# Optimization experiments

Measured on AMD Instinct MI355X. Metric: run time of the kernel, lower is better.

## Reference

```python
import jax, jax.numpy as jnp
import numpy as np

B, X_DIM, Y_DIM, HIDDEN = 512, 768, 128, 1024
H2 = HIDDEN // 2


def setup_inputs() -> dict:
    key = jax.random.key(0)
    ks = jax.random.split(key, 10)
    s_in = 1.0 / np.sqrt(X_DIM)
    s_h = 1.0 / np.sqrt(H2)
    return {
        "x_samples": jax.random.normal(ks[0], (B, X_DIM), jnp.float32),
        "y_samples": jax.random.normal(ks[1], (B, Y_DIM), jnp.float32),
        "w1_mu": jax.random.uniform(ks[2], (X_DIM, H2), jnp.float32, -s_in, s_in),
        "b1_mu": jax.random.uniform(ks[3], (H2,), jnp.float32, -s_in, s_in),
        "w2_mu": jax.random.uniform(ks[4], (H2, Y_DIM), jnp.float32, -s_h, s_h),
        "b2_mu": jax.random.uniform(ks[5], (Y_DIM,), jnp.float32, -s_h, s_h),
        "w1_lv": jax.random.uniform(ks[6], (X_DIM, H2), jnp.float32, -s_in, s_in),
        "b1_lv": jax.random.uniform(ks[7], (H2,), jnp.float32, -s_in, s_in),
        "w2_lv": jax.random.uniform(ks[8], (H2, Y_DIM), jnp.float32, -s_h, s_h),
        "b2_lv": jax.random.uniform(ks[9], (Y_DIM,), jnp.float32, -s_h, s_h),
    }


def reference(x_samples, y_samples, w1_mu, b1_mu, w2_mu, b2_mu,
              w1_lv, b1_lv, w2_lv, b2_lv):
    batch = y_samples.shape[0]
    # p_mu / p_logvar MLP heads
    mu = jax.nn.relu(x_samples @ w1_mu + b1_mu) @ w2_mu + b2_mu          # [B, Y]
    logvar = jnp.tanh(jax.nn.relu(x_samples @ w1_lv + b1_lv) @ w2_lv + b2_lv)  # [B, Y]

    inv_var = jnp.exp(-logvar)
    # positive: diagonal Gaussian log-prob of y_i under p(.|x_i), up to const
    positive = (-0.5 * (mu - y_samples) ** 2 * inv_var - 0.5 * logvar).sum(-1)  # [B]

    # pairwise log-probs: row i = params from x_i, col j = sample y_j
    mu_1 = mu[:, None, :]            # [B, 1, Y]
    lv_1 = logvar[:, None, :]        # [B, 1, Y]
    y_1 = y_samples[None, :, :]      # [1, B, Y]
    all_probs = (-0.5 * (y_1 - mu_1) ** 2 * jnp.exp(-lv_1) - 0.5 * lv_1).sum(-1)  # [B, B]

    # Faithful replication of the torch broadcasting: diag_mask is [B, B, 1],
    # so all_probs + diag_mask broadcasts to [B, B, B], then logsumexp over dim 0.
    diag_mask = (jnp.eye(batch, dtype=all_probs.dtype) * -20.0)[:, :, None]  # [B, B, 1]
    logits = all_probs + diag_mask                                           # [B, B, B]
    negative = jax.scipy.special.logsumexp(logits, axis=0) - jnp.log(batch - 1.0)  # [B, B]

    return (positive - negative).mean()
```

## Files before the change

### kernel.cpp

```cpp
#include <hip/hip_runtime.h>
#include <math.h>

#define BSZ   512
#define XD    768
#define YD    128
#define H2D   512

__global__ __launch_bounds__(512) void ysum_kernel(
    const float* __restrict__ y, double* __restrict__ Sy,
    double* __restrict__ Sy2, double* __restrict__ accum)
{
    const int t  = threadIdx.x;
    const int dl = t & 31;
    const int g  = t >> 5;
    const int d  = blockIdx.x * 32 + dl;

    float s = 0.f, s2 = 0.f;
    for (int i = g * 32; i < g * 32 + 32; ++i) {
        const float v = y[i * YD + d];
        s += v; s2 += v * v;
    }
    __shared__ float sh[16][33];
    __shared__ float sh2[16][33];
    sh[g][dl] = s; sh2[g][dl] = s2;
    __syncthreads();
    if (t < 32) {
        double S = 0.0, S2 = 0.0;
        #pragma unroll
        for (int gg = 0; gg < 16; ++gg) { S += (double)sh[gg][t]; S2 += (double)sh2[gg][t]; }
        Sy[blockIdx.x * 32 + t]  = S;
        Sy2[blockIdx.x * 32 + t] = S2;
    } else if (blockIdx.x == 0 && t == 32) {
        accum[0] = 0.0;
    } else if (blockIdx.x == 0 && t == 33) {
        accum[1] = 0.0;
    }
}

__global__ __launch_bounds__(256, 2) void layer1_kernel(
    const float* __restrict__ x,
    const float* __restrict__ w1_mu, const float* __restrict__ b1_mu,
    const float* __restrict__ w1_lv, const float* __restrict__ b1_lv,
    float* __restrict__ h_mu, float* __restrict__ h_lv)
{
    const int which = blockIdx.z;
    const float* __restrict__ W    = which ? w1_lv : w1_mu;
    const float* __restrict__ bias = which ? b1_lv : b1_mu;
    float* __restrict__ H          = which ? h_lv  : h_mu;

    __shared__ float As[32][68];
    __shared__ float Bs[32][68];

    const int t  = threadIdx.x;
    const int m0 = blockIdx.x * 32;
    const int n0 = blockIdx.y * 32;
    const int tx = t & 15;
    const int ty = t >> 4;

    const int ar = t >> 3;
    const int ak = (t & 7) * 8;
    const int bk = t >> 2;
    const int bn = (t & 3) * 8;

    float acc00 = 0.f, acc01 = 0.f, acc10 = 0.f, acc11 = 0.f;

    for (int k0 = 0; k0 < XD; k0 += 64) {
        const float4 a_lo = *(const float4*)&x[(m0 + ar) * XD + k0 + ak];
        const float4 a_hi = *(const float4*)&x[(m0 + ar) * XD + k0 + ak + 4];
        const float4 w_lo = *(const float4*)&W[(k0 + bk) * H2D + n0 + bn];
        const float4 w_hi = *(const float4*)&W[(k0 + bk) * H2D + n0 + bn + 4];
        __syncthreads();
        *(float4*)&As[ar][ak]     = a_lo;
        *(float4*)&As[ar][ak + 4] = a_hi;
        Bs[bn + 0][bk] = w_lo.x; Bs[bn + 1][bk] = w_lo.y;
        Bs[bn + 2][bk] = w_lo.z; Bs[bn + 3][bk] = w_lo.w;
        Bs[bn + 4][bk] = w_hi.x; Bs[bn + 5][bk] = w_hi.y;
        Bs[bn + 6][bk] = w_hi.z; Bs[bn + 7][bk] = w_hi.w;
        __syncthreads();
        #pragma unroll
        for (int k = 0; k < 64; k += 4) {
            const float4 a0 = *(const float4*)&As[ty][k];
            const float4 a1 = *(const float4*)&As[ty + 16][k];
            const float4 b0 = *(const float4*)&Bs[tx][k];
            const float4 b1 = *(const float4*)&Bs[tx + 16][k];
            acc00 += a0.x*b0.x; acc00 += a0.y*b0.y; acc00 += a0.z*b0.z; acc00 += a0.w*b0.w;
            acc01 += a0.x*b1.x; acc01 += a0.y*b1.y; acc01 += a0.z*b1.z; acc01 += a0.w*b1.w;
            acc10 += a1.x*b0.x; acc10 += a1.y*b0.y; acc10 += a1.z*b0.z; acc10 += a1.w*b0.w;
            acc11 += a1.x*b1.x; acc11 += a1.y*b1.y; acc11 += a1.z*b1.z; acc11 += a1.w*b1.w;
        }
    }

    const int na = n0 + tx, nb = n0 + tx + 16;
    const float ba = bias[na], bb = bias[nb];
    H[(m0 + ty)      * H2D + na] = fmaxf(acc00 + ba, 0.f);
    H[(m0 + ty)      * H2D + nb] = fmaxf(acc01 + bb, 0.f);
    H[(m0 + ty + 16) * H2D + na] = fmaxf(acc10 + ba, 0.f);
    H[(m0 + ty + 16) * H2D + nb] = fmaxf(acc11 + bb, 0.f);
}

__global__ __launch_bounds__(256, 2) void layer2p_kernel(
    const float* __restrict__ h_mu, const float* __restrict__ h_lv,
    const float* __restrict__ w2_mu, const float* __restrict__ w2_lv,
    float* __restrict__ part)
{
    const int branch = blockIdx.z >> 2;
    const int kz     = blockIdx.z & 3;
    const float* __restrict__ A = branch ? h_lv  : h_mu;
    const float* __restrict__ W = branch ? w2_lv : w2_mu;
    float* __restrict__ out = part + (size_t)blockIdx.z * (BSZ * YD);

    __shared__ float As[32][68];
    __shared__ float Bs[32][68];

    const int t  = threadIdx.x;
    const int m0 = blockIdx.x * 32;
    const int n0 = blockIdx.y * 32;
    const int tx = t & 15;
    const int ty = t >> 4;

    const int ar = t >> 3;
    const int ak = (t & 7) * 8;
    const int bk = t >> 2;
    const int bn = (t & 3) * 8;

    float acc00 = 0.f, acc01 = 0.f, acc10 = 0.f, acc11 = 0.f;

    const int kbase = kz * 128;
    for (int k0 = kbase; k0 < kbase + 128; k0 += 64) {
        const float4 a_lo = *(const float4*)&A[(m0 + ar) * H2D + k0 + ak];
        const float4 a_hi = *(const float4*)&A[(m0 + ar) * H2D + k0 + ak + 4];
        const float4 w_lo = *(const float4*)&W[(k0 + bk) * YD + n0 + bn];
        const float4 w_hi = *(const float4*)&W[(k0 + bk) * YD + n0 + bn + 4];
        __syncthreads();
        *(float4*)&As[ar][ak]     = a_lo;
        *(float4*)&As[ar][ak + 4] = a_hi;
        Bs[bn + 0][bk] = w_lo.x; Bs[bn + 1][bk] = w_lo.y;
        Bs[bn + 2][bk] = w_lo.z; Bs[bn + 3][bk] = w_lo.w;
        Bs[bn + 4][bk] = w_hi.x; Bs[bn + 5][bk] = w_hi.y;
        Bs[bn + 6][bk] = w_hi.z; Bs[bn + 7][bk] = w_hi.w;
        __syncthreads();
        #pragma unroll
        for (int k = 0; k < 64; k += 4) {
            const float4 a0 = *(const float4*)&As[ty][k];
            const float4 a1 = *(const float4*)&As[ty + 16][k];
            const float4 b0 = *(const float4*)&Bs[tx][k];
            const float4 b1 = *(const float4*)&Bs[tx + 16][k];
            acc00 += a0.x*b0.x; acc00 += a0.y*b0.y; acc00 += a0.z*b0.z; acc00 += a0.w*b0.w;
            acc01 += a0.x*b1.x; acc01 += a0.y*b1.y; acc01 += a0.z*b1.z; acc01 += a0.w*b1.w;
            acc10 += a1.x*b0.x; acc10 += a1.y*b0.y; acc10 += a1.z*b0.z; acc10 += a1.w*b0.w;
            acc11 += a1.x*b1.x; acc11 += a1.y*b1.y; acc11 += a1.z*b1.z; acc11 += a1.w*b1.w;
        }
    }

    out[(m0 + ty)      * YD + n0 + tx]      = acc00;
    out[(m0 + ty)      * YD + n0 + tx + 16] = acc01;
    out[(m0 + ty + 16) * YD + n0 + tx]      = acc10;
    out[(m0 + ty + 16) * YD + n0 + tx + 16] = acc11;
}

__global__ __launch_bounds__(256) void reduce_kernel(
    const float* __restrict__ part, const float* __restrict__ y,
    const float* __restrict__ b2_mu, const float* __restrict__ b2_lv,
    const double* __restrict__ Sy, const double* __restrict__ Sy2,
    double* __restrict__ accum)
{
    const int NE = BSZ * YD;
    double pos = 0.0, ap = 0.0;
    for (int e = blockIdx.x * 256 + threadIdx.x; e < NE; e += 128 * 256) {
        const int d = e & (YD - 1);
        const float mu = part[0 * NE + e] + part[1 * NE + e]
                       + part[2 * NE + e] + part[3 * NE + e] + b2_mu[d];
        const float lvp = part[4 * NE + e] + part[5 * NE + e]
                        + part[6 * NE + e] + part[7 * NE + e] + b2_lv[d];
        const float lv = tanhf(lvp);
        const float iv = expf(-lv);
        const float dm = mu - y[e];
        pos += -0.5 * (double)dm * (double)dm * (double)iv - 0.5 * (double)lv;
        ap  += (double)iv * (-0.5 * Sy2[d] + (double)mu * Sy[d]
                             - 0.5 * (double)BSZ * (double)mu * (double)mu)
             - 0.5 * (double)BSZ * (double)lv;
    }
    #pragma unroll
    for (int off = 32; off > 0; off >>= 1) {
        pos += __shfl_down(pos, off);
        ap  += __shfl_down(ap, off);
    }
    __shared__ double sp[4];
    __shared__ double sa[4];
    const int lane = threadIdx.x & 63;
    const int wv   = threadIdx.x >> 6;
    if (lane == 0) { sp[wv] = pos; sa[wv] = ap; }
    __syncthreads();
    if (threadIdx.x == 0) {
        atomicAdd(&accum[0], sp[0] + sp[1] + sp[2] + sp[3]);
        atomicAdd(&accum[1], sa[0] + sa[1] + sa[2] + sa[3]);
    }
}

__global__ void finalize_kernel(const double* __restrict__ accum,
                                float* __restrict__ out)
{
    if (threadIdx.x == 0) {
        const double C = log1p(exp(-20.0) / (double)(BSZ - 1));
        out[0] = (float)(accum[0] / (double)BSZ
                       - accum[1] / ((double)BSZ * (double)BSZ) - C);
    }
}

extern "C" void kernel_launch(void* const* d_in, const int* in_sizes, int n_in,
                              void* d_out, int out_size, void* d_ws, size_t ws_size,
                              hipStream_t stream) {
    const float* x     = (const float*)d_in[0];
    const float* y     = (const float*)d_in[1];
    const float* w1_mu = (const float*)d_in[2];
    const float* b1_mu = (const float*)d_in[3];
    const float* w2_mu = (const float*)d_in[4];
    const float* b2_mu = (const float*)d_in[5];
    const float* w1_lv = (const float*)d_in[6];
    const float* b1_lv = (const float*)d_in[7];
    const float* w2_lv = (const float*)d_in[8];
    const float* b2_lv = (const float*)d_in[9];

    char* ws = (char*)d_ws;
    float*  h_mu  = (float*)(ws);
    float*  h_lv  = (float*)(ws + (size_t)BSZ * H2D * 4);
    float*  part  = (float*)(ws + (size_t)2 * BSZ * H2D * 4);
    double* Sy    = (double*)(ws + (size_t)2 * BSZ * H2D * 4
                                 + (size_t)8 * BSZ * YD * 4);
    double* Sy2   = Sy + YD;
    double* accum = Sy2 + YD;

    ysum_kernel<<<4, 512, 0, stream>>>(y, Sy, Sy2, accum);
    layer1_kernel<<<dim3(16, 16, 2), 256, 0, stream>>>(
        x, w1_mu, b1_mu, w1_lv, b1_lv, h_mu, h_lv);
    layer2p_kernel<<<dim3(16, 4, 8), 256, 0, stream>>>(
        h_mu, h_lv, w2_mu, w2_lv, part);
    reduce_kernel<<<128, 256, 0, stream>>>(
        part, y, b2_mu, b2_lv, Sy, Sy2, accum);
    finalize_kernel<<<1, 64, 0, stream>>>(accum, (float*)d_out);
}
```

Measured before the change: 117.6 us.

## Fuse ysum into layer1, split-K layer1, 64x64 register tiles, last-block finalize

```diff
diff --git a/kernel.cpp b/kernel.cpp
--- a/kernel.cpp
+++ b/kernel.cpp
@@ -6,180 +6,195 @@
 #define YD    128
 #define H2D   512
 
-__global__ __launch_bounds__(512) void ysum_kernel(
-    const float* __restrict__ y, double* __restrict__ Sy,
-    double* __restrict__ Sy2, double* __restrict__ accum)
-{
-    const int t  = threadIdx.x;
-    const int dl = t & 31;
-    const int g  = t >> 5;
-    const int d  = blockIdx.x * 32 + dl;
-
-    float s = 0.f, s2 = 0.f;
-    for (int i = g * 32; i < g * 32 + 32; ++i) {
-        const float v = y[i * YD + d];
-        s += v; s2 += v * v;
-    }
-    __shared__ float sh[16][33];
-    __shared__ float sh2[16][33];
-    sh[g][dl] = s; sh2[g][dl] = s2;
-    __syncthreads();
-    if (t < 32) {
-        double S = 0.0, S2 = 0.0;
-        #pragma unroll
-        for (int gg = 0; gg < 16; ++gg) { S += (double)sh[gg][t]; S2 += (double)sh2[gg][t]; }
-        Sy[blockIdx.x * 32 + t]  = S;
-        Sy2[blockIdx.x * 32 + t] = S2;
-    } else if (blockIdx.x == 0 && t == 32) {
-        accum[0] = 0.0;
-    } else if (blockIdx.x == 0 && t == 33) {
-        accum[1] = 0.0;
-    }
-}
-
 __global__ __launch_bounds__(256, 2) void layer1_kernel(
     const float* __restrict__ x,
-    const float* __restrict__ w1_mu, const float* __restrict__ b1_mu,
-    const float* __restrict__ w1_lv, const float* __restrict__ b1_lv,
-    float* __restrict__ h_mu, float* __restrict__ h_lv)
+    const float* __restrict__ w1_mu, const float* __restrict__ w1_lv,
+    const float* __restrict__ y,
+    float* __restrict__ p1,
+    double* __restrict__ Sy, double* __restrict__ Sy2,
+    double* __restrict__ accum, unsigned int* __restrict__ counter)
 {
-    const int which = blockIdx.z;
-    const float* __restrict__ W    = which ? w1_lv : w1_mu;
-    const float* __restrict__ bias = which ? b1_lv : b1_mu;
-    float* __restrict__ H          = which ? h_lv  : h_mu;
-
-    __shared__ float As[32][68];
-    __shared__ float Bs[32][68];
-
-    const int t  = threadIdx.x;
-    const int m0 = blockIdx.x * 32;
-    const int n0 = blockIdx.y * 32;
+    __shared__ float As[16][68];
+    __shared__ float Bs[16][68];
+    const int t = threadIdx.x;
+
+    if (blockIdx.z == 4) {
+        const int id = blockIdx.x + 8 * blockIdx.y;
+        if (id >= 16) return;
+        const int dl = t & 7;
+        const int g  = t >> 3;
+        const int d  = id * 8 + dl;
+        float s = 0.f, s2 = 0.f;
+        for (int i = g * 16; i < g * 16 + 16; ++i) {
+            const float v = y[i * YD + d];
+            s += v; s2 += v * v;
+        }
+        float* shs  = &As[0][0];
+        float* shs2 = &Bs[0][0];
+        shs[t] = s; shs2[t] = s2;
+        __syncthreads();
+        if (t < 8) {
+            double S = 0.0, S2 = 0.0;
+            #pragma unroll
+            for (int gg = 0; gg < 32; ++gg) {
+                S += (double)shs[gg * 8 + t]; S2 += (double)shs2[gg * 8 + t];
+            }
+            Sy[id * 8 + t] = S; Sy2[id * 8 + t] = S2;
+        } else if (id == 0 && t == 8)  { accum[0] = 0.0; }
+        else if (id == 0 && t == 9)  { accum[1] = 0.0; }
+        else if (id == 0 && t == 10) { *counter = 0u; }
+        return;
+    }
+
+    const int bz     = blockIdx.z;
+    const int branch = bz >> 1;
+    const int ks     = bz & 1;
+    const float* __restrict__ W = branch ? w1_lv : w1_mu;
+    float* __restrict__ out = p1 + (size_t)bz * (BSZ * H2D);
+
+    const int m0 = blockIdx.x * 64;
+    const int n0 = blockIdx.y * 64;
     const int tx = t & 15;
     const int ty = t >> 4;
 
-    const int ar = t >> 3;
-    const int ak = (t & 7) * 8;
-    const int bk = t >> 2;
-    const int bn = (t & 3) * 8;
-
-    float acc00 = 0.f, acc01 = 0.f, acc10 = 0.f, acc11 = 0.f;
-
-    for (int k0 = 0; k0 < XD; k0 += 64) {
-        const float4 a_lo = *(const float4*)&x[(m0 + ar) * XD + k0 + ak];
-        const float4 a_hi = *(const float4*)&x[(m0 + ar) * XD + k0 + ak + 4];
-        const float4 w_lo = *(const float4*)&W[(k0 + bk) * H2D + n0 + bn];
-        const float4 w_hi = *(const float4*)&W[(k0 + bk) * H2D + n0 + bn + 4];
-        __syncthreads();
-        *(float4*)&As[ar][ak]     = a_lo;
-        *(float4*)&As[ar][ak + 4] = a_hi;
-        Bs[bn + 0][bk] = w_lo.x; Bs[bn + 1][bk] = w_lo.y;
-        Bs[bn + 2][bk] = w_lo.z; Bs[bn + 3][bk] = w_lo.w;
-        Bs[bn + 4][bk] = w_hi.x; Bs[bn + 5][bk] = w_hi.y;
-        Bs[bn + 6][bk] = w_hi.z; Bs[bn + 7][bk] = w_hi.w;
-        __syncthreads();
+    const int am  = t >> 2;
+    const int akq = (t & 3) << 2;
+    const int bkk = t >> 4;
+    const int bnq = (t & 15) << 2;
+
+    const int kbase = ks * 384;
+    float acc[4][4] = {};
+
+    float4 a_pref = *(const float4*)&x[(m0 + am) * XD + kbase + akq];
+    float4 b_pref = *(const float4*)&W[(kbase + bkk) * H2D + n0 + bnq];
+
+    for (int kt = 0; kt < 384; kt += 16) {
+        __syncthreads();
+        As[akq + 0][am] = a_pref.x;
+        As[akq + 1][am] = a_pref.y;
+        As[akq + 2][am] = a_pref.z;
+        As[akq + 3][am] = a_pref.w;
+        *(float4*)&Bs[bkk][bnq] = b_pref;
+        __syncthreads();
+        if (kt + 16 < 384) {
+            const int kn = kbase + kt + 16;
+            a_pref = *(const float4*)&x[(m0 + am) * XD + kn + akq];
+            b_pref = *(const float4*)&W[(kn + bkk) * H2D + n0 + bnq];
+        }
         #pragma unroll
-        for (int k = 0; k < 64; k += 4) {
-            const float4 a0 = *(const float4*)&As[ty][k];
-            const float4 a1 = *(const float4*)&As[ty + 16][k];
-            const float4 b0 = *(const float4*)&Bs[tx][k];
-            const float4 b1 = *(const float4*)&Bs[tx + 16][k];
-            acc00 += a0.x*b0.x; acc00 += a0.y*b0.y; acc00 += a0.z*b0.z; acc00 += a0.w*b0.w;
-            acc01 += a0.x*b1.x; acc01 += a0.y*b1.y; acc01 += a0.z*b1.z; acc01 += a0.w*b1.w;
-            acc10 += a1.x*b0.x; acc10 += a1.y*b0.y; acc10 += a1.z*b0.z; acc10 += a1.w*b0.w;
-            acc11 += a1.x*b1.x; acc11 += a1.y*b1.y; acc11 += a1.z*b1.z; acc11 += a1.w*b1.w;
-        }
-    }
-
-    const int na = n0 + tx, nb = n0 + tx + 16;
-    const float ba = bias[na], bb = bias[nb];
-    H[(m0 + ty)      * H2D + na] = fmaxf(acc00 + ba, 0.f);
-    H[(m0 + ty)      * H2D + nb] = fmaxf(acc01 + bb, 0.f);
-    H[(m0 + ty + 16) * H2D + na] = fmaxf(acc10 + ba, 0.f);
-    H[(m0 + ty + 16) * H2D + nb] = fmaxf(acc11 + bb, 0.f);
-}
-
-__global__ __launch_bounds__(256, 2) void layer2p_kernel(
-    const float* __restrict__ h_mu, const float* __restrict__ h_lv,
+        for (int k = 0; k < 16; ++k) {
+            const float4 av = *(const float4*)&As[k][ty * 4];
+            const float4 bv = *(const float4*)&Bs[k][tx * 4];
+            acc[0][0] += av.x*bv.x; acc[0][1] += av.x*bv.y; acc[0][2] += av.x*bv.z; acc[0][3] += av.x*bv.w;
+            acc[1][0] += av.y*bv.x; acc[1][1] += av.y*bv.y; acc[1][2] += av.y*bv.z; acc[1][3] += av.y*bv.w;
+            acc[2][0] += av.z*bv.x; acc[2][1] += av.z*bv.y; acc[2][2] += av.z*bv.z; acc[2][3] += av.z*bv.w;
+            acc[3][0] += av.w*bv.x; acc[3][1] += av.w*bv.y; acc[3][2] += av.w*bv.z; acc[3][3] += av.w*bv.w;
+        }
+    }
+
+    #pragma unroll
+    for (int i = 0; i < 4; ++i) {
+        const float4 o = make_float4(acc[i][0], acc[i][1], acc[i][2], acc[i][3]);
+        *(float4*)&out[(m0 + ty * 4 + i) * H2D + n0 + tx * 4] = o;
+    }
+}
+
+__global__ __launch_bounds__(256, 2) void layer2_kernel(
+    const float* __restrict__ p1,
+    const float* __restrict__ b1_mu, const float* __restrict__ b1_lv,
     const float* __restrict__ w2_mu, const float* __restrict__ w2_lv,
-    float* __restrict__ part)
+    float* __restrict__ p2)
 {
-    const int branch = blockIdx.z >> 2;
-    const int kz     = blockIdx.z & 3;
-    const float* __restrict__ A = branch ? h_lv  : h_mu;
-    const float* __restrict__ W = branch ? w2_lv : w2_mu;
-    float* __restrict__ out = part + (size_t)blockIdx.z * (BSZ * YD);
-
-    __shared__ float As[32][68];
-    __shared__ float Bs[32][68];
-
-    const int t  = threadIdx.x;
-    const int m0 = blockIdx.x * 32;
-    const int n0 = blockIdx.y * 32;
+    __shared__ float As[16][68];
+    __shared__ float Bs[16][68];
+    const int t = threadIdx.x;
+
+    const int branch = blockIdx.z >> 3;
+    const int ks     = blockIdx.z & 7;
+    const float* __restrict__ pa = p1 + (size_t)(branch * 2 + 0) * (BSZ * H2D);
+    const float* __restrict__ pb = p1 + (size_t)(branch * 2 + 1) * (BSZ * H2D);
+    const float* __restrict__ b1 = branch ? b1_lv : b1_mu;
+    const float* __restrict__ W  = branch ? w2_lv : w2_mu;
+    float* __restrict__ out = p2 + (size_t)blockIdx.z * (BSZ * YD);
+
+    const int m0 = blockIdx.x * 64;
+    const int n0 = blockIdx.y * 64;
     const int tx = t & 15;
     const int ty = t >> 4;
 
-    const int ar = t >> 3;
-    const int ak = (t & 7) * 8;
-    const int bk = t >> 2;
-    const int bn = (t & 3) * 8;
-
-    float acc00 = 0.f, acc01 = 0.f, acc10 = 0.f, acc11 = 0.f;
-
-    const int kbase = kz * 128;
-    for (int k0 = kbase; k0 < kbase + 128; k0 += 64) {
-        const float4 a_lo = *(const float4*)&A[(m0 + ar) * H2D + k0 + ak];
-        const float4 a_hi = *(const float4*)&A[(m0 + ar) * H2D + k0 + ak + 4];
-        const float4 w_lo = *(const float4*)&W[(k0 + bk) * YD + n0 + bn];
-        const float4 w_hi = *(const float4*)&W[(k0 + bk) * YD + n0 + bn + 4];
-        __syncthreads();
-        *(float4*)&As[ar][ak]     = a_lo;
-        *(float4*)&As[ar][ak + 4] = a_hi;
-        Bs[bn + 0][bk] = w_lo.x; Bs[bn + 1][bk] = w_lo.y;
-        Bs[bn + 2][bk] = w_lo.z; Bs[bn + 3][bk] = w_lo.w;
-        Bs[bn + 4][bk] = w_hi.x; Bs[bn + 5][bk] = w_hi.y;
-        Bs[bn + 6][bk] = w_hi.z; Bs[bn + 7][bk] = w_hi.w;
-        __syncthreads();
+    const int am  = t >> 2;
+    const int akq = (t & 3) << 2;
+    const int bkk = t >> 4;
+    const int bnq = (t & 15) << 2;
+
+    const int kbase = ks * 64;
+    float acc[4][4] = {};
+
+    float4 pa4 = *(const float4*)&pa[(m0 + am) * H2D + kbase + akq];
+    float4 pb4 = *(const float4*)&pb[(m0 + am) * H2D + kbase + akq];
+    float4 bb4 = *(const float4*)&b1[kbase + akq];
+    float4 w4  = *(const float4*)&W[(kbase + bkk) * YD + n0 + bnq];
+
+    for (int kt = 0; kt < 64; kt += 16) {
+        __syncthreads();
+        As[akq + 0][am] = fmaxf(pa4.x + pb4.x + bb4.x, 0.f);
+        As[akq + 1][am] = fmaxf(pa4.y + pb4.y + bb4.y, 0.f);
+        As[akq + 2][am] = fmaxf(pa4.z + pb4.z + bb4.z, 0.f);
+        As[akq + 3][am] = fmaxf(pa4.w + pb4.w + bb4.w, 0.f);
+        *(float4*)&Bs[bkk][bnq] = w4;
+        __syncthreads();
+        if (kt + 16 < 64) {
+            const int kn = kbase + kt + 16;
+            pa4 = *(const float4*)&pa[(m0 + am) * H2D + kn + akq];
+            pb4 = *(const float4*)&pb[(m0 + am) * H2D + kn + akq];
+            bb4 = *(const float4*)&b1[kn + akq];
+            w4  = *(const float4*)&W[(kn + bkk) * YD + n0 + bnq];
+        }
         #pragma unroll
-        for (int k = 0; k < 64; k += 4) {
-            const float4 a0 = *(const float4*)&As[ty][k];
-            const float4 a1 = *(const float4*)&As[ty + 16][k];
-            const float4 b0 = *(const float4*)&Bs[tx][k];
-            const float4 b1 = *(const float4*)&Bs[tx + 16][k];
-            acc00 += a0.x*b0.x; acc00 += a0.y*b0.y; acc00 += a0.z*b0.z; acc00 += a0.w*b0.w;
-            acc01 += a0.x*b1.x; acc01 += a0.y*b1.y; acc01 += a0.z*b1.z; acc01 += a0.w*b1.w;
-            acc10 += a1.x*b0.x; acc10 += a1.y*b0.y; acc10 += a1.z*b0.z; acc10 += a1.w*b0.w;
-            acc11 += a1.x*b1.x; acc11 += a1.y*b1.y; acc11 += a1.z*b1.z; acc11 += a1.w*b1.w;
-        }
-    }
-
-    out[(m0 + ty)      * YD + n0 + tx]      = acc00;
-    out[(m0 + ty)      * YD + n0 + tx + 16] = acc01;
-    out[(m0 + ty + 16) * YD + n0 + tx]      = acc10;
-    out[(m0 + ty + 16) * YD + n0 + tx + 16] = acc11;
+        for (int k = 0; k < 16; ++k) {
+            const float4 av = *(const float4*)&As[k][ty * 4];
+            const float4 bv = *(const float4*)&Bs[k][tx * 4];
+            acc[0][0] += av.x*bv.x; acc[0][1] += av.x*bv.y; acc[0][2] += av.x*bv.z; acc[0][3] += av.x*bv.w;
+            acc[1][0] += av.y*bv.x; acc[1][1] += av.y*bv.y; acc[1][2] += av.y*bv.z; acc[1][3] += av.y*bv.w;
+            acc[2][0] += av.z*bv.x; acc[2][1] += av.z*bv.y; acc[2][2] += av.z*bv.z; acc[2][3] += av.z*bv.w;
+            acc[3][0] += av.w*bv.x; acc[3][1] += av.w*bv.y; acc[3][2] += av.w*bv.z; acc[3][3] += av.w*bv.w;
+        }
+    }
+
+    #pragma unroll
+    for (int i = 0; i < 4; ++i) {
+        const float4 o = make_float4(acc[i][0], acc[i][1], acc[i][2], acc[i][3]);
+        *(float4*)&out[(m0 + ty * 4 + i) * YD + n0 + tx * 4] = o;
+    }
 }
 
 __global__ __launch_bounds__(256) void reduce_kernel(
-    const float* __restrict__ part, const float* __restrict__ y,
+    const float* __restrict__ p2, const float* __restrict__ y,
     const float* __restrict__ b2_mu, const float* __restrict__ b2_lv,
     const double* __restrict__ Sy, const double* __restrict__ Sy2,
-    double* __restrict__ accum)
+    double* __restrict__ accum, unsigned int* __restrict__ counter,
+    float* __restrict__ outp)
 {
     const int NE = BSZ * YD;
-    double pos = 0.0, ap = 0.0;
-    for (int e = blockIdx.x * 256 + threadIdx.x; e < NE; e += 128 * 256) {
-        const int d = e & (YD - 1);
-        const float mu = part[0 * NE + e] + part[1 * NE + e]
-                       + part[2 * NE + e] + part[3 * NE + e] + b2_mu[d];
-        const float lvp = part[4 * NE + e] + part[5 * NE + e]
-                        + part[6 * NE + e] + part[7 * NE + e] + b2_lv[d];
-        const float lv = tanhf(lvp);
-        const float iv = expf(-lv);
-        const float dm = mu - y[e];
-        pos += -0.5 * (double)dm * (double)dm * (double)iv - 0.5 * (double)lv;
-        ap  += (double)iv * (-0.5 * Sy2[d] + (double)mu * Sy[d]
-                             - 0.5 * (double)BSZ * (double)mu * (double)mu)
-             - 0.5 * (double)BSZ * (double)lv;
-    }
+    const int e  = blockIdx.x * 256 + threadIdx.x;
+    const int d  = e & (YD - 1);
+
+    float mu = b2_mu[d];
+    float lp = b2_lv[d];
+    #pragma unroll
+    for (int s = 0; s < 8; ++s) {
+        mu += p2[s * NE + e];
+        lp += p2[(8 + s) * NE + e];
+    }
+    const float lv = tanhf(lp);
+    const float iv = expf(-lv);
+    const float dm = mu - y[e];
+
+    double pos = -0.5 * (double)dm * (double)dm * (double)iv - 0.5 * (double)lv;
+    double ap  = (double)iv * (-0.5 * Sy2[d] + (double)mu * Sy[d]
+                               - 256.0 * (double)mu * (double)mu)
+               - 256.0 * (double)lv;
+
     #pragma unroll
     for (int off = 32; off > 0; off >>= 1) {
         pos += __shfl_down(pos, off);
@@ -194,16 +209,14 @@
     if (threadIdx.x == 0) {
         atomicAdd(&accum[0], sp[0] + sp[1] + sp[2] + sp[3]);
         atomicAdd(&accum[1], sa[0] + sa[1] + sa[2] + sa[3]);
-    }
-}
-
-__global__ void finalize_kernel(const double* __restrict__ accum,
-                                float* __restrict__ out)
-{
-    if (threadIdx.x == 0) {
-        const double C = log1p(exp(-20.0) / (double)(BSZ - 1));
-        out[0] = (float)(accum[0] / (double)BSZ
-                       - accum[1] / ((double)BSZ * (double)BSZ) - C);
+        __threadfence();
+        const unsigned int old = atomicAdd(counter, 1u);
+        if (old == 255u) {
+            const double P = atomicAdd(&accum[0], 0.0);
+            const double A = atomicAdd(&accum[1], 0.0);
+            const double C = log1p(exp(-20.0) / 511.0);
+            outp[0] = (float)(P / 512.0 - A / 262144.0 - C);
+        }
     }
 }
 
@@ -222,20 +235,18 @@
     const float* b2_lv = (const float*)d_in[9];
 
     char* ws = (char*)d_ws;
-    float*  h_mu  = (float*)(ws);
-    float*  h_lv  = (float*)(ws + (size_t)BSZ * H2D * 4);
-    float*  part  = (float*)(ws + (size_t)2 * BSZ * H2D * 4);
-    double* Sy    = (double*)(ws + (size_t)2 * BSZ * H2D * 4
-                                 + (size_t)8 * BSZ * YD * 4);
-    double* Sy2   = Sy + YD;
+    float*  p1 = (float*)(ws);
+    float*  p2 = (float*)(ws + (size_t)4 * BSZ * H2D * 4);
+    double* Sy = (double*)(ws + (size_t)4 * BSZ * H2D * 4
+                              + (size_t)16 * BSZ * YD * 4);
+    double* Sy2 = Sy + YD;
     double* accum = Sy2 + YD;
-
-    ysum_kernel<<<4, 512, 0, stream>>>(y, Sy, Sy2, accum);
-    layer1_kernel<<<dim3(16, 16, 2), 256, 0, stream>>>(
-        x, w1_mu, b1_mu, w1_lv, b1_lv, h_mu, h_lv);
-    layer2p_kernel<<<dim3(16, 4, 8), 256, 0, stream>>>(
-        h_mu, h_lv, w2_mu, w2_lv, part);
-    reduce_kernel<<<128, 256, 0, stream>>>(
-        part, y, b2_mu, b2_lv, Sy, Sy2, accum);
-    finalize_kernel<<<1, 64, 0, stream>>>(accum, (float*)d_out);
-}
+    unsigned int* counter = (unsigned int*)(accum + 2);
+
+    layer1_kernel<<<dim3(8, 8, 5), 256, 0, stream>>>(
+        x, w1_mu, w1_lv, y, p1, Sy, Sy2, accum, counter);
+    layer2_kernel<<<dim3(8, 2, 16), 256, 0, stream>>>(
+        p1, b1_mu, b1_lv, w2_mu, w2_lv, p2);
+    reduce_kernel<<<256, 256, 0, stream>>>(
+        p2, y, b2_mu, b2_lv, Sy, Sy2, accum, counter, (float*)d_out);
+}
```

New measurement: 109.6 us. -6.8%, faster.
